# Kernel optimization log

Hardware: AMD Instinct MI355X
Metric: run time of the kernel (lower is better)

The kernel has to match this reference:

```python
import jax, jax.numpy as jnp
import numpy as np

B, N, C, M, OUT = 4, 256, 32, 4, 64


def _uniform(k, shape, fan_in):
    s = 1.0 / np.sqrt(fan_in)
    return jax.random.uniform(k, shape, jnp.float32, -s, s)


def setup_inputs() -> dict:
    key = jax.random.key(0)
    ks = jax.random.split(key, 11)
    return {
        "x": jax.random.normal(ks[0], (B, N, N, C), jnp.float32),
        # Neighborhood / SnConv2to1 linears (in=C, out=M neighborhood channels)
        "w1_nb": _uniform(ks[1], (3 * C, M), 3 * C),
        "b1_nb": _uniform(ks[2], (M,), 3 * C),
        "w0_nb": _uniform(ks[3], (2 * C, M), 2 * C),
        "b0_nb": _uniform(ks[4], (M,), 2 * C),
        # SnConv2 linears (in channels = M*C after neighborhood product)
        "w2d": _uniform(ks[5], (2 * M * C, OUT), 2 * M * C),
        "b2d": _uniform(ks[6], (OUT,), 2 * M * C),
        "w1d": _uniform(ks[7], (3 * M * C, OUT), 3 * M * C),
        "b1d": _uniform(ks[8], (OUT,), 3 * M * C),
        "w0d": _uniform(ks[9], (2 * M * C, OUT), 2 * M * C),
        "b0d": _uniform(ks[10], (OUT,), 2 * M * C),
    }


def _contractions(x):
    # x: [B, n, n, c]; mask=None, reduction='mean' path of _get_contractions
    n = x.shape[1]
    rowsum = x.sum(axis=1) / n                      # [B, n, c]
    colsum = x.sum(axis=2) / n                      # [B, n, c]
    diag = jnp.diagonal(x, axis1=1, axis2=2)        # [B, c, n]
    rowcolsum = x.sum(axis=(1, 2)) / (n * n)        # [B, c]
    diag_sum = diag.sum(axis=-1) / n                # [B, c]  (/= sqrt(n^2))
    diag = jnp.moveaxis(diag, -1, 1)                # move_from_end -> [B, n, c]
    return rowsum, colsum, diag, rowcolsum, diag_sum


def reference(x, w1_nb, b1_nb, w0_nb, b0_nb, w2d, b2d, w1d, b1d, w0d, b0d):
    # ---- Neighborhood: SnConv2to1 -> sigmoid ----
    rs, cs, dg, rcs, ds = _contractions(x)
    obj1 = jnp.concatenate([rs, cs, dg], axis=-1)             # [B, n, 3C]
    obj0 = jnp.concatenate([rcs, ds], axis=-1)                # [B, 2C]
    node = obj1 @ w1_nb + b1_nb + (obj0 @ w0_nb + b0_nb)[:, None, :]
    neighbs = jax.nn.sigmoid(node)                            # [B, n, M]
    # ---- _neighbor_elementwise_product ----
    expanded = neighbs[:, None, :, :] * neighbs[:, :, None, :]  # [B, n, n, M]
    # channel_product: outer product over channel dims, collapsed to M*C
    xl = (expanded[..., :, None] * x[..., None, :]).reshape(B, N, N, M * C)
    # ---- SnConv2 on the localized tensor ----
    rs2, cs2, dg2, rcs2, ds2 = _contractions(xl)
    obj2d = jnp.concatenate([xl, jnp.swapaxes(xl, 1, 2)], axis=-1)  # [B,n,n,2MC]
    obj1d = jnp.concatenate([rs2, cs2, dg2], axis=-1)               # [B,n,3MC]
    obj0d = jnp.concatenate([rcs2, ds2], axis=-1)                   # [B,2MC]
    out = (obj2d @ w2d + b2d
           + (obj1d @ w1d + b1d)[:, None, :, :]
           + (obj0d @ w0d + b0d)[:, None, None, :])                 # [B,n,n,OUT]
    return out
```

## Files before the change

### kernel.cpp

```cpp
#include <hip/hip_runtime.h>
#include <math.h>

#define Bv 4
#define Nv 256
#define Cv 32
#define Mv 4
#define OUTv 64
#define MCv (Mv*Cv)

typedef _Float16 h8 __attribute__((ext_vector_type(8)));
typedef _Float16 h4 __attribute__((ext_vector_type(4)));
typedef float f4 __attribute__((ext_vector_type(4)));

__device__ __align__(16) float g_rs  [Bv * Nv * Cv];
__device__ __align__(16) float g_cs  [Bv * Nv * Cv];
__device__ __align__(16) float g_dgx [Bv * Nv * Cv];
__device__ __align__(16) float g_nb  [Bv * Nv * Mv];
__device__ __align__(16) float g_rcs2R[8 * Bv * MCv];
__device__ __align__(16) float g_ds2R [8 * Bv * MCv];
__device__ __align__(16) float g_addv[Bv * Nv * OUTv];
__device__ __align__(16) _Float16 g_wfrag[8 * 4 * 64 * 8];

__global__ __launch_bounds__(256) void k_contract1(const float* __restrict__ x,
                                                   const float* __restrict__ w2d) {
    int bx = blockIdx.x, b = blockIdx.y;
    int t = threadIdx.x;
    if (bx >= 2 * Nv) {
        if (b != 0) return;
        int r = bx - 2 * Nv;
        if (r == 8) {
            float4 z = {0.f,0.f,0.f,0.f};
            #pragma unroll
            for (int k = 0; k < 4; k++) {
                ((float4*)g_rcs2R)[k * 256 + t] = z;
                ((float4*)g_ds2R )[k * 256 + t] = z;
            }
            return;
        }
        int fi = r * 256 + t;
        int s = fi >> 8, q = (fi >> 6) & 3, lane = fi & 63;
        int k0 = s * 32 + ((lane >> 4) << 3);
        int o = q * 16 + (lane & 15);
        #pragma unroll
        for (int jj = 0; jj < 8; jj++)
            g_wfrag[fi * 8 + jj] = (_Float16)w2d[(size_t)(k0 + jj) * OUTv + o];
        return;
    }
    int c4 = t & 7, sub = t >> 3;
    const float4* xb4 = (const float4*)(x + (size_t)b * Nv * Nv * Cv);
    __shared__ float red[32][36];
    float4 acc = {0.f,0.f,0.f,0.f};
    if (bx < Nv) {
        int n = bx;
        for (int i = sub; i < Nv; i += 32) {
            float4 v = xb4[((size_t)i * Nv + n) * 8 + c4];
            acc.x += v.x; acc.y += v.y; acc.z += v.z; acc.w += v.w;
        }
        red[sub][c4*4+0] = acc.x; red[sub][c4*4+1] = acc.y;
        red[sub][c4*4+2] = acc.z; red[sub][c4*4+3] = acc.w;
        __syncthreads();
        if (t < 32) {
            float s = 0.f;
            #pragma unroll
            for (int k = 0; k < 32; k++) s += red[k][t];
            g_rs[(b * Nv + n) * Cv + t] = s * (1.0f / Nv);
        }
        if (t < 8) ((float4*)g_dgx)[(b * Nv + n) * 8 + t] = xb4[((size_t)n * Nv + n) * 8 + t];
    } else {
        int n = bx - Nv;
        for (int j = sub; j < Nv; j += 32) {
            float4 v = xb4[((size_t)n * Nv + j) * 8 + c4];
            acc.x += v.x; acc.y += v.y; acc.z += v.z; acc.w += v.w;
        }
        red[sub][c4*4+0] = acc.x; red[sub][c4*4+1] = acc.y;
        red[sub][c4*4+2] = acc.z; red[sub][c4*4+3] = acc.w;
        __syncthreads();
        if (t < 32) {
            float s = 0.f;
            #pragma unroll
            for (int k = 0; k < 32; k++) s += red[k][t];
            g_cs[(b * Nv + n) * Cv + t] = s * (1.0f / Nv);
        }
    }
}

__global__ void k_neighb(const float* __restrict__ w1, const float* __restrict__ b1,
                         const float* __restrict__ w0, const float* __restrict__ b0) {
    int b = blockIdx.x, t = threadIdx.x;
    int c = t & 31, sub = t >> 5;
    float ar = 0.f, ad = 0.f;
    for (int n = sub; n < Nv; n += 8) {
        ar += g_rs[(b * Nv + n) * Cv + c];
        ad += g_dgx[(b * Nv + n) * Cv + c];
    }
    __shared__ float red[8][64];
    __shared__ float obj0[64];
    __shared__ float redm[64][4];
    __shared__ float t0nb[4];
    red[sub][c] = ar;
    red[sub][32 + c] = ad;
    __syncthreads();
    if (t < 64) {
        float s = 0.f;
        #pragma unroll
        for (int k = 0; k < 8; k++) s += red[k][t];
        obj0[t] = s * (1.0f / Nv);
    }
    __syncthreads();
    {
        int k = t >> 2, m = t & 3;
        redm[k][m] = obj0[k] * w0[k * Mv + m];
    }
    __syncthreads();
    if (t < 4) {
        float v = b0[t];
        #pragma unroll
        for (int k = 0; k < 64; k++) v += redm[k][t];
        t0nb[t] = v;
    }
    __syncthreads();
    int n = t;
    float node[4];
    #pragma unroll
    for (int m = 0; m < 4; m++) node[m] = t0nb[m] + b1[m];
    for (int cc = 0; cc < Cv; cc++) {
        float r = g_rs[(b * Nv + n) * Cv + cc];
        float s = g_cs[(b * Nv + n) * Cv + cc];
        float d = g_dgx[(b * Nv + n) * Cv + cc];
        #pragma unroll
        for (int m = 0; m < 4; m++)
            node[m] += r * w1[cc * Mv + m] + s * w1[(Cv + cc) * Mv + m] + d * w1[(2 * Cv + cc) * Mv + m];
    }
    #pragma unroll
    for (int m = 0; m < 4; m++)
        g_nb[(b * Nv + n) * Mv + m] = 1.0f / (1.0f + expf(-node[m]));
}

__global__ __launch_bounds__(256) void k_fused(const float* __restrict__ x,
    const float* __restrict__ w1d, const float* __restrict__ b1d,
    const float* __restrict__ b2d, const float* __restrict__ b0d) {
    int n = blockIdx.x, b = blockIdx.y;
    int t = threadIdx.x;

    __shared__ __align__(16) float4 nb4[Nv];
    __shared__ float red[2][16][132];
    __shared__ float S1l[MCv], S2l[MCv];
    __shared__ float redD[4][64];

    nb4[t] = ((const float4*)g_nb)[b * Nv + t];
    __syncthreads();

    const float4* xb4 = (const float4*)(x + (size_t)b * Nv * Nv * Cv);
    int half = t >> 7, tt = t & 127, c4 = tt & 7, sub = tt >> 3;
    float4 a[4];
    #pragma unroll
    for (int m = 0; m < 4; m++) a[m] = {0.f,0.f,0.f,0.f};
    for (int i = sub; i < Nv; i += 16) {
        float4 v = half ? xb4[((size_t)n * Nv + i) * 8 + c4]
                        : xb4[((size_t)i * Nv + n) * 8 + c4];
        float4 nv = nb4[i];
        a[0].x += nv.x*v.x; a[0].y += nv.x*v.y; a[0].z += nv.x*v.z; a[0].w += nv.x*v.w;
        a[1].x += nv.y*v.x; a[1].y += nv.y*v.y; a[1].z += nv.y*v.z; a[1].w += nv.y*v.w;
        a[2].x += nv.z*v.x; a[2].y += nv.z*v.y; a[2].z += nv.z*v.z; a[2].w += nv.z*v.w;
        a[3].x += nv.w*v.x; a[3].y += nv.w*v.y; a[3].z += nv.w*v.z; a[3].w += nv.w*v.w;
    }
    #pragma unroll
    for (int m = 0; m < 4; m++) {
        red[half][sub][m*32 + c4*4+0] = a[m].x; red[half][sub][m*32 + c4*4+1] = a[m].y;
        red[half][sub][m*32 + c4*4+2] = a[m].z; red[half][sub][m*32 + c4*4+3] = a[m].w;
    }
    __syncthreads();
    if (t < 128) {
        float s = 0.f;
        #pragma unroll
        for (int k = 0; k < 16; k++) s += red[0][k][t];
        S1l[t] = s;
        int m = t >> 5, c = t & 31;
        float nv = ((const float*)&nb4[n])[m];
        int rep = ((n & 7) * Bv + b) * MCv + t;
        atomicAdd(&g_rcs2R[rep], nv * s);
        atomicAdd(&g_ds2R [rep], nv * nv * g_dgx[(b * Nv + n) * Cv + c]);
    } else {
        int u = t - 128;
        float s = 0.f;
        #pragma unroll
        for (int k = 0; k < 16; k++) s += red[1][k][u];
        S2l[u] = s;
    }
    __syncthreads();

    {
        int o = t & 63, ks = t >> 6;
        const float invN = 1.0f / Nv;
        float nv = ((const float*)&nb4[n])[ks];
        float f = nv * invN, d2 = nv * nv;
        const float* dgr = g_dgx + (size_t)(b * Nv + n) * Cv;
        float acc = 0.f;
        #pragma unroll 8
        for (int cc = 0; cc < 32; cc++) {
            int mc = ks * 32 + cc;
            acc += f * S1l[mc] * w1d[(size_t)mc * OUTv + o]
                 + f * S2l[mc] * w1d[(size_t)(MCv + mc) * OUTv + o]
                 + d2 * dgr[cc] * w1d[(size_t)(2 * MCv + mc) * OUTv + o];
        }
        redD[ks][o] = acc;
    }
    __syncthreads();
    if (t < 64) {
        float v = redD[0][t] + redD[1][t] + redD[2][t] + redD[3][t]
                + b1d[t] + b2d[t] + b0d[t];
        g_addv[(size_t)(b * Nv + n) * OUTv + t] = v;
    }
}

#define XPAD 40
__global__ __launch_bounds__(256) void k_main(const float* __restrict__ x,
                                              float* __restrict__ out,
                                              const float* __restrict__ w0d) {
    int jt = blockIdx.x, ip = blockIdx.y, b = blockIdx.z;
    int i0 = ip * 2, i1 = i0 + 1;
    int j0 = jt * 128;
    int t = threadIdx.x;
    int lane = t & 63, w = t >> 6;
    int rowA = lane & 15, quad = lane >> 4;

    __shared__ __align__(16) _Float16 Wl[8 * 4 * 64 * 8];
    __shared__ __align__(16) _Float16 Xt0[128 * XPAD];
    __shared__ __align__(16) _Float16 Xb0[128 * XPAD];
    __shared__ __align__(16) _Float16 Xt1[128 * XPAD];
    __shared__ __align__(16) _Float16 Xb1[128 * XPAD];
    __shared__ float rcl[MCv], dsl[MCv];
    __shared__ float t0red[4][64];
    __shared__ float t0l[64];

    {
        const float4* src = (const float4*)g_wfrag;
        float4* dst = (float4*)Wl;
        #pragma unroll
        for (int r = 0; r < 8; r++) dst[r * 256 + t] = src[r * 256 + t];
    }
    {
        const float4* x4 = (const float4*)x;
        #pragma unroll
        for (int r = 0; r < 4; r++) {
            int idx = r * 256 + t;
            int j = idx >> 3, c4 = idx & 7;
            float4 v0 = x4[((size_t)(b * Nv + i0) * Nv + j0 + j) * 8 + c4];
            float4 v1 = x4[((size_t)(b * Nv + i1) * Nv + j0 + j) * 8 + c4];
            float4 u0 = x4[((size_t)(b * Nv + j0 + j) * Nv + i0) * 8 + c4];
            float4 u1 = x4[((size_t)(b * Nv + j0 + j) * Nv + i1) * 8 + c4];
            h4 h0; h0[0] = (_Float16)v0.x; h0[1] = (_Float16)v0.y;
            h0[2] = (_Float16)v0.z; h0[3] = (_Float16)v0.w;
            *(h4*)&Xt0[j * XPAD + c4 * 4] = h0;
            h4 h1; h1[0] = (_Float16)v1.x; h1[1] = (_Float16)v1.y;
            h1[2] = (_Float16)v1.z; h1[3] = (_Float16)v1.w;
            *(h4*)&Xt1[j * XPAD + c4 * 4] = h1;
            h4 g0; g0[0] = (_Float16)u0.x; g0[1] = (_Float16)u0.y;
            g0[2] = (_Float16)u0.z; g0[3] = (_Float16)u0.w;
            *(h4*)&Xb0[j * XPAD + c4 * 4] = g0;
            h4 g1; g1[0] = (_Float16)u1.x; g1[1] = (_Float16)u1.y;
            g1[2] = (_Float16)u1.z; g1[3] = (_Float16)u1.w;
            *(h4*)&Xb1[j * XPAD + c4 * 4] = g1;
        }
    }
    if (t < 128) {
        float s = 0.f;
        #pragma unroll
        for (int r = 0; r < 8; r++) s += g_rcs2R[(r * Bv + b) * MCv + t];
        rcl[t] = s;
    } else {
        int tt = t - 128;
        float s = 0.f;
        #pragma unroll
        for (int r = 0; r < 8; r++) s += g_ds2R[(r * Bv + b) * MCv + tt];
        dsl[tt] = s;
    }
    int jl1 = w * 32 + rowA, jl2 = jl1 + 16;
    _Float16 e1h0[4], e2h0[4], e1h1[4], e2h1[4];
    {
        const float* ni0 = g_nb + (size_t)(b * Nv + i0) * Mv;
        const float* ni1 = g_nb + (size_t)(b * Nv + i1) * Mv;
        const float* n1 = g_nb + (size_t)(b * Nv + j0 + jl1) * Mv;
        const float* n2 = g_nb + (size_t)(b * Nv + j0 + jl2) * Mv;
        #pragma unroll
        for (int m = 0; m < 4; m++) {
            e1h0[m] = (_Float16)(ni0[m] * n1[m]);
            e2h0[m] = (_Float16)(ni0[m] * n2[m]);
            e1h1[m] = (_Float16)(ni1[m] * n1[m]);
            e2h1[m] = (_Float16)(ni1[m] * n2[m]);
        }
    }
    __syncthreads();
    {
        int o = t & 63, ks = t >> 6;
        const float invN = 1.0f / Nv;
        const float invN2 = invN * invN;
        float a0 = 0.f;
        #pragma unroll 8
        for (int cc = 0; cc < 32; cc++) {
            int mc = ks * 32 + cc;
            a0 += invN2 * rcl[mc] * w0d[(size_t)mc * OUTv + o]
                + invN  * dsl[mc] * w0d[(size_t)(MCv + mc) * OUTv + o];
        }
        t0red[ks][o] = a0;
    }
    __syncthreads();
    if (t < 64) t0l[t] = t0red[0][t] + t0red[1][t] + t0red[2][t] + t0red[3][t];
    __syncthreads();

    f4 acc[2][2][4];
    #pragma unroll
    for (int ii = 0; ii < 2; ii++)
        #pragma unroll
        for (int js = 0; js < 2; js++)
            #pragma unroll
            for (int q = 0; q < 4; q++) acc[ii][js][q] = {0.f, 0.f, 0.f, 0.f};

    const h8* Wf = (const h8*)Wl;
    #pragma unroll
    for (int part = 0; part < 2; part++) {
        const _Float16* X0 = part ? Xb0 : Xt0;
        const _Float16* X1 = part ? Xb1 : Xt1;
        h8 xv1_0 = *(const h8*)&X0[jl1 * XPAD + quad * 8];
        h8 xv2_0 = *(const h8*)&X0[jl2 * XPAD + quad * 8];
        h8 xv1_1 = *(const h8*)&X1[jl1 * XPAD + quad * 8];
        h8 xv2_1 = *(const h8*)&X1[jl2 * XPAD + quad * 8];
        #pragma unroll
        for (int m = 0; m < 4; m++) {
            h8 a1_0 = xv1_0 * e1h0[m];
            h8 a2_0 = xv2_0 * e2h0[m];
            h8 a1_1 = xv1_1 * e1h1[m];
            h8 a2_1 = xv2_1 * e2h1[m];
            int s = part * 4 + m;
            #pragma unroll
            for (int q = 0; q < 4; q++) {
                h8 bf = Wf[(s * 4 + q) * 64 + lane];
                acc[0][0][q] = __builtin_amdgcn_mfma_f32_16x16x32_f16(a1_0, bf, acc[0][0][q], 0, 0, 0);
                acc[0][1][q] = __builtin_amdgcn_mfma_f32_16x16x32_f16(a2_0, bf, acc[0][1][q], 0, 0, 0);
                acc[1][0][q] = __builtin_amdgcn_mfma_f32_16x16x32_f16(a1_1, bf, acc[1][0][q], 0, 0, 0);
                acc[1][1][q] = __builtin_amdgcn_mfma_f32_16x16x32_f16(a2_1, bf, acc[1][1][q], 0, 0, 0);
            }
        }
    }
    #pragma unroll
    for (int js = 0; js < 2; js++) {
        int jbase = j0 + w * 32 + js * 16 + quad * 4;
        #pragma unroll
        for (int q = 0; q < 4; q++) {
            int o = q * 16 + rowA;
            float tv = t0l[o];
            #pragma unroll
            for (int r = 0; r < 4; r++) {
                int j = jbase + r;
                float av = g_addv[(size_t)(b * Nv + j) * OUTv + o] + tv;
                out[(((size_t)(b * Nv + i0)) * Nv + j) * OUTv + o] = acc[0][js][q][r] + av;
                out[(((size_t)(b * Nv + i1)) * Nv + j) * OUTv + o] = acc[1][js][q][r] + av;
            }
        }
    }
}

extern "C" void kernel_launch(void* const* d_in, const int* in_sizes, int n_in,
                              void* d_out, int out_size, void* d_ws, size_t ws_size,
                              hipStream_t stream) {
    const float* x     = (const float*)d_in[0];
    const float* w1_nb = (const float*)d_in[1];
    const float* b1_nb = (const float*)d_in[2];
    const float* w0_nb = (const float*)d_in[3];
    const float* b0_nb = (const float*)d_in[4];
    const float* w2d   = (const float*)d_in[5];
    const float* b2d   = (const float*)d_in[6];
    const float* w1d   = (const float*)d_in[7];
    const float* b1d   = (const float*)d_in[8];
    const float* w0d   = (const float*)d_in[9];
    const float* b0d   = (const float*)d_in[10];
    float* out = (float*)d_out;
    (void)d_ws; (void)ws_size;

    hipLaunchKernelGGL(k_contract1, dim3(2 * Nv + 9, Bv), dim3(256), 0, stream, x, w2d);
    hipLaunchKernelGGL(k_neighb, dim3(Bv), dim3(256), 0, stream,
                       w1_nb, b1_nb, w0_nb, b0_nb);
    hipLaunchKernelGGL(k_fused, dim3(Nv, Bv), dim3(256), 0, stream,
                       x, w1d, b1d, b2d, b0d);
    hipLaunchKernelGGL(k_main, dim3(2, Nv / 2, Bv), dim3(256), 0, stream, x, out, w0d);
}
```

Measured before the change: 167.3 us.

## Fuse row and column sums into a single pass with projected partials

The first contraction kernel used to read x twice: one set of blocks did strided row sums and another did column sums. Now each block walks 4 rows once. It writes the per-row sums, and it accumulates the per-block column sums already multiplied by the rowsum slice of w1_nb into small partial tensors. The neighborhood kernel then adds these 64 partials instead of reading a full rowsum array, and it takes the global mean from the column sums. This roughly halves the traffic over x in that stage. In exchange the grid shrinks to far fewer, heavier blocks with large shared-memory use, which may hide memory latency less well.

```diff
diff --git a/kernel.cpp b/kernel.cpp
--- a/kernel.cpp
+++ b/kernel.cpp
@@ -12,22 +12,23 @@
 typedef _Float16 h4 __attribute__((ext_vector_type(4)));
 typedef float f4 __attribute__((ext_vector_type(4)));
 
-__device__ __align__(16) float g_rs  [Bv * Nv * Cv];
 __device__ __align__(16) float g_cs  [Bv * Nv * Cv];
 __device__ __align__(16) float g_dgx [Bv * Nv * Cv];
 __device__ __align__(16) float g_nb  [Bv * Nv * Mv];
+__device__ __align__(16) float g_rwP [Bv * 64 * Nv * Mv];
 __device__ __align__(16) float g_rcs2R[8 * Bv * MCv];
 __device__ __align__(16) float g_ds2R [8 * Bv * MCv];
 __device__ __align__(16) float g_addv[Bv * Nv * OUTv];
 __device__ __align__(16) _Float16 g_wfrag[8 * 4 * 64 * 8];
 
 __global__ __launch_bounds__(256) void k_contract1(const float* __restrict__ x,
-                                                   const float* __restrict__ w2d) {
+                                                   const float* __restrict__ w2d,
+                                                   const float* __restrict__ w1) {
     int bx = blockIdx.x, b = blockIdx.y;
     int t = threadIdx.x;
-    if (bx >= 2 * Nv) {
+    if (bx >= 64) {
         if (b != 0) return;
-        int r = bx - 2 * Nv;
+        int r = bx - 64;
         if (r == 8) {
             float4 z = {0.f,0.f,0.f,0.f};
             #pragma unroll
@@ -46,41 +47,75 @@
             g_wfrag[fi * 8 + jj] = (_Float16)w2d[(size_t)(k0 + jj) * OUTv + o];
         return;
     }
-    int c4 = t & 7, sub = t >> 3;
+    int c4 = t & 7, jb = t >> 3;
+    int i0 = bx * 4;
     const float4* xb4 = (const float4*)(x + (size_t)b * Nv * Nv * Cv);
-    __shared__ float red[32][36];
-    float4 acc = {0.f,0.f,0.f,0.f};
-    if (bx < Nv) {
-        int n = bx;
-        for (int i = sub; i < Nv; i += 32) {
-            float4 v = xb4[((size_t)i * Nv + n) * 8 + c4];
-            acc.x += v.x; acc.y += v.y; acc.z += v.z; acc.w += v.w;
-        }
-        red[sub][c4*4+0] = acc.x; red[sub][c4*4+1] = acc.y;
-        red[sub][c4*4+2] = acc.z; red[sub][c4*4+3] = acc.w;
+    __shared__ __align__(16) float4 red2[32][8];
+    __shared__ float redw[256][36];
+
+    float4 acc8[8];
+    #pragma unroll
+    for (int k = 0; k < 8; k++) acc8[k] = {0.f,0.f,0.f,0.f};
+
+    for (int r = 0; r < 4; r++) {
+        int i = i0 + r;
+        float4 v[8];
+        #pragma unroll
+        for (int k = 0; k < 8; k++)
+            v[k] = xb4[((size_t)i * Nv + jb + 32 * k) * 8 + c4];
+        float4 rsum = {0.f,0.f,0.f,0.f};
+        #pragma unroll
+        for (int k = 0; k < 8; k++) {
+            acc8[k].x += v[k].x; acc8[k].y += v[k].y;
+            acc8[k].z += v[k].z; acc8[k].w += v[k].w;
+            rsum.x += v[k].x; rsum.y += v[k].y;
+            rsum.z += v[k].z; rsum.w += v[k].w;
+        }
+        red2[jb][c4] = rsum;
         __syncthreads();
-        if (t < 32) {
+        if (t < 8) {
+            float4 s = {0.f,0.f,0.f,0.f};
+            #pragma unroll
+            for (int k2 = 0; k2 < 32; k2++) {
+                float4 u = red2[k2][t];
+                s.x += u.x; s.y += u.y; s.z += u.z; s.w += u.w;
+            }
+            const float sc = 1.0f / Nv;
+            s.x *= sc; s.y *= sc; s.z *= sc; s.w *= sc;
+            ((float4*)g_cs)[(b * Nv + i) * 8 + t] = s;
+        }
+        __syncthreads();
+    }
+    if (t < 8) {
+        #pragma unroll
+        for (int r = 0; r < 4; r++) {
+            int i = i0 + r;
+            ((float4*)g_dgx)[(b * Nv + i) * 8 + t] = xb4[((size_t)i * Nv + i) * 8 + t];
+        }
+    }
+    #pragma unroll
+    for (int k = 0; k < 8; k++) {
+        int j = jb + 32 * k;
+        #pragma unroll
+        for (int m = 0; m < 4; m++) {
+            float wc = acc8[k].x * w1[(c4 * 4 + 0) * Mv + m]
+                     + acc8[k].y * w1[(c4 * 4 + 1) * Mv + m]
+                     + acc8[k].z * w1[(c4 * 4 + 2) * Mv + m]
+                     + acc8[k].w * w1[(c4 * 4 + 3) * Mv + m];
+            redw[j][c4 * 4 + m] = wc;
+        }
+    }
+    __syncthreads();
+    {
+        float4 rw;
+        #pragma unroll
+        for (int m = 0; m < 4; m++) {
             float s = 0.f;
             #pragma unroll
-            for (int k = 0; k < 32; k++) s += red[k][t];
-            g_rs[(b * Nv + n) * Cv + t] = s * (1.0f / Nv);
-        }
-        if (t < 8) ((float4*)g_dgx)[(b * Nv + n) * 8 + t] = xb4[((size_t)n * Nv + n) * 8 + t];
-    } else {
-        int n = bx - Nv;
-        for (int j = sub; j < Nv; j += 32) {
-            float4 v = xb4[((size_t)n * Nv + j) * 8 + c4];
-            acc.x += v.x; acc.y += v.y; acc.z += v.z; acc.w += v.w;
-        }
-        red[sub][c4*4+0] = acc.x; red[sub][c4*4+1] = acc.y;
-        red[sub][c4*4+2] = acc.z; red[sub][c4*4+3] = acc.w;
-        __syncthreads();
-        if (t < 32) {
-            float s = 0.f;
-            #pragma unroll
-            for (int k = 0; k < 32; k++) s += red[k][t];
-            g_cs[(b * Nv + n) * Cv + t] = s * (1.0f / Nv);
-        }
+            for (int q = 0; q < 8; q++) s += redw[t][q * 4 + m];
+            ((float*)&rw)[m] = s;
+        }
+        ((float4*)g_rwP)[((size_t)b * 64 + bx) * Nv + t] = rw;
     }
 }
 
@@ -90,7 +125,7 @@
     int c = t & 31, sub = t >> 5;
     float ar = 0.f, ad = 0.f;
     for (int n = sub; n < Nv; n += 8) {
-        ar += g_rs[(b * Nv + n) * Cv + c];
+        ar += g_cs[(b * Nv + n) * Cv + c];
         ad += g_dgx[(b * Nv + n) * Cv + c];
     }
     __shared__ float red[8][64];
@@ -120,16 +155,21 @@
     }
     __syncthreads();
     int n = t;
+    float4 rwv = {0.f,0.f,0.f,0.f};
+    for (int g = 0; g < 64; g++) {
+        float4 p = ((const float4*)g_rwP)[((size_t)b * 64 + g) * Nv + n];
+        rwv.x += p.x; rwv.y += p.y; rwv.z += p.z; rwv.w += p.w;
+    }
     float node[4];
     #pragma unroll
-    for (int m = 0; m < 4; m++) node[m] = t0nb[m] + b1[m];
+    for (int m = 0; m < 4; m++)
+        node[m] = t0nb[m] + b1[m] + ((float*)&rwv)[m] * (1.0f / Nv);
     for (int cc = 0; cc < Cv; cc++) {
-        float r = g_rs[(b * Nv + n) * Cv + cc];
         float s = g_cs[(b * Nv + n) * Cv + cc];
         float d = g_dgx[(b * Nv + n) * Cv + cc];
         #pragma unroll
         for (int m = 0; m < 4; m++)
-            node[m] += r * w1[cc * Mv + m] + s * w1[(Cv + cc) * Mv + m] + d * w1[(2 * Cv + cc) * Mv + m];
+            node[m] += s * w1[(Cv + cc) * Mv + m] + d * w1[(2 * Cv + cc) * Mv + m];
     }
     #pragma unroll
     for (int m = 0; m < 4; m++)
@@ -377,7 +417,8 @@
     float* out = (float*)d_out;
     (void)d_ws; (void)ws_size;
 
-    hipLaunchKernelGGL(k_contract1, dim3(2 * Nv + 9, Bv), dim3(256), 0, stream, x, w2d);
+    hipLaunchKernelGGL(k_contract1, dim3(64 + 9, Bv), dim3(256), 0, stream,
+                       x, w2d, w1_nb);
     hipLaunchKernelGGL(k_neighb, dim3(Bv), dim3(256), 0, stream,
                        w1_nb, b1_nb, w0_nb, b0_nb);
     hipLaunchKernelGGL(k_fused, dim3(Nv, Bv), dim3(256), 0, stream,
```

Result: no change. 168.8 us (+0.9%).
